# Optimization experiments

Measured on AMD Instinct MI355X. Metric: run time of the kernel, lower is better.

The kernel has to match this reference:

```python
import jax, jax.numpy as jnp
import numpy as np

B, S, N = 16, 512, 321          # batch, input length, n_variates (dec_in)
D, DF, LAYERS = 512, 2048, 2    # d_model, d_ff, e_layers
M, K, P = 3, 3, 96              # wavelet levels, kernel_size, pred_len
ALPHA = 0.3


def _dwconv(x, h, dilation):
    # x: [B, C, L], h: [C, K] depthwise dilated conv (cross-correlation, like torch)
    return jax.lax.conv_general_dilated(
        x, h[:, None, :], window_strides=(1,), padding='VALID',
        rhs_dilation=(dilation,), dimension_numbers=('NCH', 'OIH', 'NCH'),
        feature_group_count=x.shape[1])


def _swt_dec(x, h0, h1):
    # stationary wavelet decomposition; x: [B, N, D] -> [B, N, M+1, D]
    approx, coeffs, dil = x, [], 1
    for _ in range(M):
        pad_total = dil * (K - 1)
        pad_r = (K * dil) // 2
        xp = jnp.pad(approx, ((0, 0), (0, 0), (pad_total - pad_r, pad_r)), mode='wrap')
        coeffs.append(_dwconv(xp, h1, dil))
        approx = _dwconv(xp, h0, dil)
        dil *= 2
    coeffs.append(approx)
    return jnp.stack(coeffs[::-1], axis=-2)


def _swt_rec(c, g0, g1):
    # inverse SWT; c: [B, N, M+1, D] -> [B, N, D]
    approx = c[:, :, 0, :]
    dil = 2 ** (M - 1)
    for i in range(M):
        det = c[:, :, 1 + i, :]
        pad_total = dil * (K - 1)
        pad_l = (dil * K) // 2
        pads = ((0, 0), (0, 0), (pad_l, pad_total - pad_l))
        approx = (_dwconv(jnp.pad(approx, pads, mode='wrap'), g0, dil)
                  + _dwconv(jnp.pad(det, pads, mode='wrap'), g1, dil)) / 2
        dil //= 2
    return approx


def _geom_attention(q, k, v):
    # q,k,v: [B, L=D, H=M+1, E=N]
    scale = 1.0 / jnp.sqrt(jnp.float32(q.shape[-1]))
    dot = jnp.einsum('blhe,bshe->bhls', q, k)
    qn2 = jnp.sum(q * q, -1).transpose(0, 2, 1)  # [B,H,L]
    kn2 = jnp.sum(k * k, -1).transpose(0, 2, 1)  # [B,H,S]
    wedge = jnp.sqrt(jax.nn.relu(qn2[:, :, :, None] * kn2[:, :, None, :] - dot * dot) + 1e-8)
    scores = ((1.0 - ALPHA) * dot + ALPHA * wedge) * scale
    A = jax.nn.softmax(scores, axis=-1)
    return jnp.einsum('bhls,bshd->blhd', A, v)


def _layernorm(x, g, b, eps=1e-5):
    mu = x.mean(-1, keepdims=True)
    var = jnp.mean((x - mu) ** 2, -1, keepdims=True)
    return (x - mu) / jnp.sqrt(var + eps) * g + b


def _forward(x_enc, emb_W, emb_b, h0, h1, g0, g1, Wq, bq, Wk, bk, Wv, bv, Wo, bo,
             W1, b1, W2, b2, ln1_g, ln1_b, ln2_g, ln2_b, lnf_g, lnf_b, proj_W, proj_b):
    # RevIN-style normalize (means detached as in torch code)
    means = jax.lax.stop_gradient(x_enc.mean(1, keepdims=True))
    stdev = jnp.sqrt(x_enc.var(1, keepdims=True) + 1e-5)
    x = (x_enc - means) / stdev
    # inverted embedding: each variate's full series -> d_model token
    h = jnp.einsum('bsn,ds->bnd', x, emb_W) + emb_b  # [B,N,D]
    for l in range(LAYERS):
        coeffs = _swt_dec(h, h0[l], h1[l])  # [B,N,M+1,D]
        q = (jnp.einsum('bnmd,ed->bnme', coeffs, Wq[l]) + bq[l]).transpose(0, 3, 2, 1)
        kk = (jnp.einsum('bnmd,ed->bnme', coeffs, Wk[l]) + bk[l]).transpose(0, 3, 2, 1)
        vv = (jnp.einsum('bnmd,ed->bnme', coeffs, Wv[l]) + bv[l]).transpose(0, 3, 2, 1)
        out = _geom_attention(q, kk, vv).transpose(0, 3, 2, 1)  # [B,N,M+1,D]
        out = _swt_rec(out, g0[l], g1[l])                        # [B,N,D]
        out = jnp.einsum('bnd,ed->bne', out, Wo[l]) + bo[l]
        x1 = _layernorm(h + out, ln1_g[l], ln1_b[l])
        y = jax.nn.gelu(jnp.einsum('bnd,fd->bnf', x1, W1[l]) + b1[l], approximate=False)
        y = jnp.einsum('bnf,df->bnd', y, W2[l]) + b2[l]
        h = _layernorm(x1 + y, ln2_g[l], ln2_b[l])
    h = _layernorm(h, lnf_g, lnf_b)
    dec = (jnp.einsum('bnd,pd->bnp', h, proj_W) + proj_b).transpose(0, 2, 1)  # [B,P,N]
    dec = dec * stdev[:, 0, :][:, None, :] + means[:, 0, :][:, None, :]
    return dec, means, stdev


def setup_inputs():
    key = jax.random.key(0)
    ks = jax.random.split(key, 24)
    def filt(k):
        f = jax.random.normal(k, (LAYERS, N, K), jnp.float32)
        return f / jnp.linalg.norm(f, axis=-1, keepdims=True)
    w = lambda k, shape: jax.random.normal(k, shape, jnp.float32) * 0.02
    z = lambda shape: jnp.zeros(shape, jnp.float32)
    o = lambda shape: jnp.ones(shape, jnp.float32)
    return {
        'x_enc': jax.random.normal(ks[0], (B, S, N), jnp.float32),
        'emb_W': w(ks[1], (D, S)), 'emb_b': z((D,)),
        'h0': filt(ks[2]), 'h1': filt(ks[3]), 'g0': filt(ks[4]), 'g1': filt(ks[5]),
        'Wq': w(ks[6], (LAYERS, D, D)), 'bq': z((LAYERS, D)),
        'Wk': w(ks[7], (LAYERS, D, D)), 'bk': z((LAYERS, D)),
        'Wv': w(ks[8], (LAYERS, D, D)), 'bv': z((LAYERS, D)),
        'Wo': w(ks[9], (LAYERS, D, D)), 'bo': z((LAYERS, D)),
        'W1': w(ks[10], (LAYERS, DF, D)), 'b1': z((LAYERS, DF)),
        'W2': w(ks[11], (LAYERS, D, DF)), 'b2': z((LAYERS, D)),
        'ln1_g': o((LAYERS, D)), 'ln1_b': z((LAYERS, D)),
        'ln2_g': o((LAYERS, D)), 'ln2_b': z((LAYERS, D)),
        'lnf_g': o((D,)), 'lnf_b': z((D,)),
        'proj_W': w(ks[12], (P, D)), 'proj_b': z((P,)),
    }


def reference(x_enc, emb_W, emb_b, h0, h1, g0, g1, Wq, bq, Wk, bk, Wv, bv, Wo, bo,
              W1, b1, W2, b2, ln1_g, ln1_b, ln2_g, ln2_b, lnf_g, lnf_b, proj_W, proj_b):
    return _forward(x_enc, emb_W, emb_b, h0, h1, g0, g1, Wq, bq, Wk, bk, Wv, bv, Wo, bo,
                    W1, b1, W2, b2, ln1_g, ln1_b, ln2_g, ln2_b, lnf_g, lnf_b, proj_W, proj_b)
```

## Files before the change

kernel.cpp:

```cpp
#include <hip/hip_runtime.h>
#include <hip/hip_bf16.h>
#include <math.h>
#include <stdint.h>

#define Bn 16
#define Sn 512
#define Nn 321
#define Dn 512
#define DFn 2048
#define Pn 96
#define KP 352

typedef __bf16 bf16x8 __attribute__((ext_vector_type(8)));
typedef float f32x4 __attribute__((ext_vector_type(4)));
typedef __hip_bfloat16 bf16;

static __device__ __forceinline__ float gelu_exact(float x) {
    return 0.5f * x * (1.0f + erff(x * 0.7071067811865476f));
}

static __device__ __forceinline__ void gld16(const void* g, void* l) {
    __builtin_amdgcn_global_load_lds(
        (const __attribute__((address_space(1))) void*)(uintptr_t)g,
        (__attribute__((address_space(3))) void*)(uintptr_t)l, 16, 0, 0);
}

struct CvtPack {
    const float* src[14];
    bf16* dst[14];
    int cnt[14];
};
__global__ void cvt_all_kernel(CvtPack p) {
    int seg = blockIdx.y;
    int n = p.cnt[seg];
    const float* s = p.src[seg];
    bf16* d = p.dst[seg];
    int i = (blockIdx.x * 256 + threadIdx.x) * 4;
    if (i + 3 < n) {
        float4 v = *reinterpret_cast<const float4*>(s + i);
        d[i] = __float2bfloat16(v.x);
        d[i + 1] = __float2bfloat16(v.y);
        d[i + 2] = __float2bfloat16(v.z);
        d[i + 3] = __float2bfloat16(v.w);
    }
}

__global__ void bias_pack_kernel(const float* __restrict__ bq, const float* __restrict__ bk,
                                 float* __restrict__ bqk) {
    int idx = blockIdx.x * 256 + threadIdx.x;
    if (idx >= 2048) return;
    int l = idx >> 10, j = idx & 1023;
    bqk[idx] = (j < 512) ? bq[l * 512 + j] : bk[l * 512 + j - 512];
}

__global__ void stats_kernel(const float* __restrict__ x, float* __restrict__ means,
                             float* __restrict__ stdev) {
    int b = blockIdx.y;
    int n = blockIdx.x * 256 + threadIdx.x;
    if (n >= Nn) return;
    const float* p = x + (size_t)b * Sn * Nn + n;
    float s = 0.f, s2 = 0.f;
    for (int ss = 0; ss < Sn; ++ss) { float v = p[(size_t)ss * Nn]; s += v; s2 += v * v; }
    float mu = s * (1.0f / Sn);
    float var = s2 * (1.0f / Sn) - mu * mu;
    means[b * Nn + n] = mu;
    stdev[b * Nn + n] = sqrtf(var + 1e-5f);
}

__global__ void transpose_norm_kernel(const float* __restrict__ x,
                                      const float* __restrict__ means,
                                      const float* __restrict__ stdev,
                                      bf16* __restrict__ xT) {
    __shared__ float tile[32][33];
    int b = blockIdx.z;
    int s0 = blockIdx.x * 32, n0 = blockIdx.y * 32;
    int tx = threadIdx.x, ty = threadIdx.y;
#pragma unroll
    for (int u = 0; u < 4; ++u) {
        int srow = ty + u * 8;
        int n = n0 + tx;
        tile[srow][tx] = (n < Nn) ? x[((size_t)b * Sn + (s0 + srow)) * Nn + n] : 0.f;
    }
    __syncthreads();
#pragma unroll
    for (int u = 0; u < 4; ++u) {
        int n = n0 + ty + u * 8;
        int s = s0 + tx;
        if (n < Nn) {
            float mu = means[b * Nn + n], sd = stdev[b * Nn + n];
            xT[((size_t)b * Nn + n) * Sn + s] = __float2bfloat16((tile[tx][ty + u * 8] - mu) / sd);
        }
    }
}

template <int OUT, int EPI>
__global__ __launch_bounds__(256) void mm_kernel(
    const bf16* __restrict__ A, const bf16* __restrict__ Bm,
    const float* __restrict__ bias, void* __restrict__ C,
    int Mdim, int Ndim, int Kdim, int lda, int ldb, int ldc,
    long sAi, long sAo, long sBi, long sBo, long sCi, long sCo, int innerB) {
    int z = blockIdx.z;
    int zi = z % innerB, zo = z / innerB;
    const bf16* Ab = A + (size_t)zi * sAi + (size_t)zo * sAo;
    const bf16* Bb = Bm + (size_t)zi * sBi + (size_t)zo * sBo;

    int gx = gridDim.x, gy = gridDim.y;
    int lin = blockIdx.y * gx + blockIdx.x;
    int prefix = (gy & ~7) * gx;
    int bx, by;
    if (lin < prefix) {
        bx = (lin >> 3) % gx;
        by = (lin / (8 * gx)) * 8 + (lin & 7);
    } else {
        int r = lin - prefix;
        bx = r % gx;
        by = (gy & ~7) + r / gx;
    }

    __shared__ __align__(16) bf16 As[2][128 * 32];
    __shared__ __align__(16) bf16 Bs[2][128 * 32];
    int t = threadIdx.x;
    int wave = t >> 6, lane = t & 63;
    int wr = wave >> 1, wc = wave & 1;
    int q = lane >> 4, l16 = lane & 15;
    int i0 = by * 128, j0 = bx * 128;

    int srow0 = t >> 2;
    int scol = (t & 3) * 8;
    f32x4 acc[4][4] = {};

    int nIter = Kdim >> 5;

    auto stage = [&](int k0, int buf) {
#pragma unroll
        for (int u = 0; u < 2; ++u) {
            int row = u * 64 + srow0;
            int gcol = scol ^ (((row >> 1) & 3) << 3);
            int gi = i0 + row; if (gi >= Mdim) gi = Mdim - 1;
            gld16(Ab + (size_t)gi * lda + k0 + gcol, &As[buf][u * 2048 + wave * 512]);
            int gj = j0 + row; if (gj >= Ndim) gj = Ndim - 1;
            gld16(Bb + (size_t)gj * ldb + k0 + gcol, &Bs[buf][u * 2048 + wave * 512]);
        }
    };

    stage(0, 0);
    for (int it = 0; it < nIter; ++it) {
        __syncthreads();
        if (it + 1 < nIter) stage((it + 1) << 5, (it + 1) & 1);
        int buf = it & 1;
        bf16x8 af[4], bfr[4];
#pragma unroll
        for (int mi = 0; mi < 4; ++mi) {
            int r = wr * 64 + mi * 16 + l16;
            int cl = (q * 8) ^ (((r >> 1) & 3) << 3);
            af[mi] = *reinterpret_cast<const bf16x8*>(&As[buf][r * 32 + cl]);
        }
#pragma unroll
        for (int ni = 0; ni < 4; ++ni) {
            int r = wc * 64 + ni * 16 + l16;
            int cl = (q * 8) ^ (((r >> 1) & 3) << 3);
            bfr[ni] = *reinterpret_cast<const bf16x8*>(&Bs[buf][r * 32 + cl]);
        }
#pragma unroll
        for (int mi = 0; mi < 4; ++mi)
#pragma unroll
            for (int ni = 0; ni < 4; ++ni)
                acc[mi][ni] = __builtin_amdgcn_mfma_f32_16x16x32_bf16(af[mi], bfr[ni], acc[mi][ni], 0, 0, 0);
    }
    size_t cbase = (size_t)zi * sCi + (size_t)zo * sCo;
#pragma unroll
    for (int mi = 0; mi < 4; ++mi) {
#pragma unroll
        for (int r = 0; r < 4; ++r) {
            int gi = i0 + wr * 64 + mi * 16 + q * 4 + r;
            if (gi >= Mdim) continue;
#pragma unroll
            for (int ni = 0; ni < 4; ++ni) {
                int gj = j0 + wc * 64 + ni * 16 + l16;
                if (gj >= Ndim) continue;
                float v = acc[mi][ni][r];
                if (bias) v += bias[gj];
                if (EPI == 1) v = gelu_exact(v);
                size_t cidx = cbase + (size_t)gi * ldc + gj;
                if (OUT == 0) ((float*)C)[cidx] = v;
                else ((bf16*)C)[cidx] = __float2bfloat16(v);
            }
        }
    }
}

__global__ __launch_bounds__(128) void swt_dec_kernel(
    const float* __restrict__ h, const float* __restrict__ h0f,
    const float* __restrict__ h1f, bf16* __restrict__ coeffs) {
    __shared__ float a[2][512];
    int b = blockIdx.y, n = blockIdx.x, t = threadIdx.x;
    const float* hrow = h + ((size_t)b * Nn + n) * Dn;
#pragma unroll
    for (int u = 0; u < 4; ++u) a[0][t + u * 128] = hrow[t + u * 128];
    float f0[3], f1[3];
#pragma unroll
    for (int k = 0; k < 3; ++k) { f0[k] = h0f[n * 3 + k]; f1[k] = h1f[n * 3 + k]; }
    __syncthreads();
    bf16* cb = coeffs + ((size_t)b * Nn + n) * 4 * Dn;
    int cur = 0;
    for (int lev = 0; lev < 3; ++lev) {
        int dil = 1 << lev;
        int pl = 2 * dil - (3 * dil) / 2;
#pragma unroll
        for (int u = 0; u < 4; ++u) {
            int d = t + u * 128;
            float dv = 0.f, av = 0.f;
#pragma unroll
            for (int k = 0; k < 3; ++k) {
                int idx = (d + k * dil - pl) & 511;
                float xv = a[cur][idx];
                dv += f1[k] * xv;
                av += f0[k] * xv;
            }
            cb[(size_t)(3 - lev) * Dn + d] = __float2bfloat16(dv);
            a[cur ^ 1][d] = av;
        }
        __syncthreads();
        cur ^= 1;
    }
#pragma unroll
    for (int u = 0; u < 4; ++u) cb[t + u * 128] = __float2bfloat16(a[cur][t + u * 128]);
}

__global__ __launch_bounds__(128) void swt_rec_kernel(
    const bf16* __restrict__ attn, const float* __restrict__ g0f,
    const float* __restrict__ g1f, bf16* __restrict__ rec) {
    __shared__ float a[2][512];
    __shared__ float det[512];
    int b = blockIdx.y, n = blockIdx.x, t = threadIdx.x;
    const bf16* base = attn + ((size_t)(b * 4) * Nn + n) * Dn;
#pragma unroll
    for (int u = 0; u < 4; ++u) a[0][t + u * 128] = __bfloat162float(base[t + u * 128]);
    float w0[3], w1[3];
#pragma unroll
    for (int k = 0; k < 3; ++k) { w0[k] = g0f[n * 3 + k]; w1[k] = g1f[n * 3 + k]; }
    int cur = 0;
    for (int i = 0; i < 3; ++i) {
        int dil = 4 >> i;
        int pl = (3 * dil) / 2;
        const bf16* drow = base + (size_t)(1 + i) * Nn * Dn;
#pragma unroll
        for (int u = 0; u < 4; ++u) det[t + u * 128] = __bfloat162float(drow[t + u * 128]);
        __syncthreads();
#pragma unroll
        for (int u = 0; u < 4; ++u) {
            int d = t + u * 128;
            float s = 0.f;
#pragma unroll
            for (int k = 0; k < 3; ++k) {
                int idx = (d + k * dil - pl) & 511;
                s += w0[k] * a[cur][idx] + w1[k] * det[idx];
            }
            a[cur ^ 1][d] = s * 0.5f;
        }
        __syncthreads();
        cur ^= 1;
    }
    bf16* out = rec + ((size_t)b * Nn + n) * Dn;
#pragma unroll
    for (int u = 0; u < 4; ++u) out[t + u * 128] = __float2bfloat16(a[cur][t + u * 128]);
}

__global__ void tconv2_kernel(const bf16* __restrict__ QK, bf16* __restrict__ QtKt) {
    __shared__ bf16 tile[32][33];
    int zz = blockIdx.z;
    int qk = zz >> 6, bm = zz & 63;
    int b = bm >> 2, m = bm & 3;
    int e0 = blockIdx.x * 32, n0 = blockIdx.y * 32;
    int tx = threadIdx.x, ty = threadIdx.y;
    const bf16* ib = QK + (size_t)b * Nn * 4096 + (size_t)m * 1024 + (size_t)qk * 512;
    bf16* ob = QtKt + (size_t)qk * 64 * 512 * KP + (size_t)bm * 512 * KP;
#pragma unroll
    for (int u = 0; u < 4; ++u) {
        int n = n0 + ty + u * 8;
        bf16 v = __float2bfloat16(0.f);
        if (n < Nn) v = ib[(size_t)n * 4096 + e0 + tx];
        tile[ty + u * 8][tx] = v;
    }
    __syncthreads();
#pragma unroll
    for (int u = 0; u < 4; ++u) {
        int e = e0 + ty + u * 8;
        int n = n0 + tx;
        if (n < KP) ob[(size_t)e * KP + n] = tile[tx][ty + u * 8];
    }
}

__global__ __launch_bounds__(256) void colsq2_kernel(const bf16* __restrict__ QK,
                                                     float* __restrict__ outv) {
    int y = blockIdx.y;
    int qk = y >> 6, bm = y & 63;
    int b = bm >> 2, m = bm & 3;
    int e0 = blockIdx.x * 64;
    int tx = threadIdx.x & 63, ty = threadIdx.x >> 6;
    const bf16* base = QK + ((size_t)b * Nn * 4 + m) * 1024 + (size_t)qk * 512;
    float s = 0.f;
    for (int n = ty; n < Nn; n += 4) {
        float v = __bfloat162float(base[(size_t)n * 4096 + e0 + tx]);
        s += v * v;
    }
    __shared__ float red[4][64];
    red[ty][tx] = s;
    __syncthreads();
    if (ty == 0)
        outv[(size_t)qk * 32768 + (size_t)bm * 512 + e0 + tx] =
            red[0][tx] + red[1][tx] + red[2][tx] + red[3][tx];
}

__global__ __launch_bounds__(256) void wedge_softmax_kernel(
    bf16* __restrict__ Smat, const float* __restrict__ qn2, const float* __restrict__ kn2) {
    int bm = blockIdx.y, l = blockIdx.x, t = threadIdx.x;
    bf16* row = Smat + ((size_t)bm * 512 + l) * 512;
    const float* kn = kn2 + (size_t)bm * 512;
    float q2 = qn2[(size_t)bm * 512 + l];
    const float scale = rsqrtf(321.0f);
    float v[2];
    float mx = -1e30f;
#pragma unroll
    for (int u = 0; u < 2; ++u) {
        int s = t + u * 256;
        float d = __bfloat162float(row[s]);
        float w = sqrtf(fmaxf(q2 * kn[s] - d * d, 0.f) + 1e-8f);
        float sc = (0.7f * d + 0.3f * w) * scale;
        v[u] = sc;
        mx = fmaxf(mx, sc);
    }
    __shared__ float red[256];
    red[t] = mx;
    __syncthreads();
    for (int o = 128; o > 0; o >>= 1) {
        if (t < o) red[t] = fmaxf(red[t], red[t + o]);
        __syncthreads();
    }
    mx = red[0];
    __syncthreads();
    float sum = 0.f;
#pragma unroll
    for (int u = 0; u < 2; ++u) {
        v[u] = expf(v[u] - mx);
        sum += v[u];
    }
    red[t] = sum;
    __syncthreads();
    for (int o = 128; o > 0; o >>= 1) {
        if (t < o) red[t] += red[t + o];
        __syncthreads();
    }
    float inv = 1.0f / red[0];
#pragma unroll
    for (int u = 0; u < 2; ++u) row[t + u * 256] = __float2bfloat16(v[u] * inv);
}

__global__ __launch_bounds__(128) void ln_kernel(
    const float* __restrict__ A, const float* __restrict__ R, const float* __restrict__ R2,
    const float* __restrict__ g, const float* __restrict__ bb,
    float* __restrict__ outf, bf16* __restrict__ outb) {
    size_t r = blockIdx.x;
    int t = threadIdx.x;
    const float* ra = A + r * Dn;
    float x[4];
    float s = 0.f, s2 = 0.f;
#pragma unroll
    for (int u = 0; u < 4; ++u) {
        int d = t + u * 128;
        float v = ra[d];
        if (R) v += R[r * Dn + d];
        if (R2) v += R2[r * Dn + d];
        x[u] = v;
        s += v;
        s2 += v * v;
    }
    __shared__ float rs[128], rs2[128];
    rs[t] = s;
    rs2[t] = s2;
    __syncthreads();
    for (int o = 64; o > 0; o >>= 1) {
        if (t < o) { rs[t] += rs[t + o]; rs2[t] += rs2[t + o]; }
        __syncthreads();
    }
    float mean = rs[0] * (1.0f / Dn);
    float var = rs2[0] * (1.0f / Dn) - mean * mean;
    float inv = rsqrtf(var + 1e-5f);
#pragma unroll
    for (int u = 0; u < 4; ++u) {
        int d = t + u * 128;
        float v = (x[u] - mean) * inv * g[d] + bb[d];
        if (outf) outf[r * Dn + d] = v;
        if (outb) outb[r * Dn + d] = __float2bfloat16(v);
    }
}

__global__ void out_scale_kernel(const float* __restrict__ ptmp,
                                 const float* __restrict__ means,
                                 const float* __restrict__ stdev, float* __restrict__ dec) {
    int idx = blockIdx.x * 256 + threadIdx.x;
    if (idx >= Bn * Pn * Nn) return;
    int n = idx % Nn;
    int bp = idx / Nn;
    int p = bp % Pn;
    int b = bp / Pn;
    const size_t PS = (size_t)Bn * Nn * Pn;
    size_t base = ((size_t)b * Nn + n) * Pn + p;
    float v = ptmp[base] + ptmp[base + PS] + ptmp[base + 2 * PS] + ptmp[base + 3 * PS];
    dec[idx] = v * stdev[b * Nn + n] + means[b * Nn + n];
}

extern "C" void kernel_launch(void* const* d_in, const int* in_sizes, int n_in,
                              void* d_out, int out_size, void* d_ws, size_t ws_size,
                              hipStream_t stream) {
    const float* x_enc = (const float*)d_in[0];
    const float* emb_W = (const float*)d_in[1];
    const float* emb_b = (const float*)d_in[2];
    const float* h0 = (const float*)d_in[3];
    const float* h1 = (const float*)d_in[4];
    const float* g0 = (const float*)d_in[5];
    const float* g1 = (const float*)d_in[6];
    const float* Wq = (const float*)d_in[7];
    const float* bq = (const float*)d_in[8];
    const float* Wk = (const float*)d_in[9];
    const float* bk = (const float*)d_in[10];
    const float* Wv = (const float*)d_in[11];
    const float* bv = (const float*)d_in[12];
    const float* Wo = (const float*)d_in[13];
    const float* bo = (const float*)d_in[14];
    const float* W1 = (const float*)d_in[15];
    const float* b1 = (const float*)d_in[16];
    const float* W2 = (const float*)d_in[17];
    const float* b2 = (const float*)d_in[18];
    const float* ln1_g = (const float*)d_in[19];
    const float* ln1_b = (const float*)d_in[20];
    const float* ln2_g = (const float*)d_in[21];
    const float* ln2_b = (const float*)d_in[22];
    const float* lnf_g = (const float*)d_in[23];
    const float* lnf_b = (const float*)d_in[24];
    const float* proj_W = (const float*)d_in[25];
    const float* proj_b = (const float*)d_in[26];

    float* dec = (float*)d_out;
    float* means = dec + (size_t)Bn * Pn * Nn;
    float* stdev = means + (size_t)Bn * Nn;

    char* p = (char*)d_ws;
    auto alloc = [&](size_t bytes) { char* r = p; p += (bytes + 255) & ~(size_t)255; return r; };
    const size_t RD = (size_t)Bn * Nn * Dn;
    const size_t RQ4 = RD * 4;

    bf16* embWb = (bf16*)alloc(262144 * 2);
    bf16* Wqkb = (bf16*)alloc(2 * 524288 * 2);
    bf16* Wvb = (bf16*)alloc(2 * 262144 * 2);
    bf16* Wob = (bf16*)alloc(2 * 262144 * 2);
    bf16* W1b = (bf16*)alloc(2 * 1048576 * 2);
    bf16* W2b = (bf16*)alloc(2 * 1048576 * 2);
    bf16* projWb = (bf16*)alloc(49152 * 2);
    float* bqk = (float*)alloc(2048 * 4);

    float* hbuf = (float*)alloc(RD * 4);
    char* regC = alloc(RQ4 * 2);
    char* regQ = alloc(RQ4 * 2);
    char* regK = alloc(RQ4 * 2);
    char* regV = alloc(RQ4 * 2);
    char* regT = alloc((size_t)2 * 64 * 512 * KP * 2);
    float* qn2 = (float*)alloc((size_t)2 * 64 * 512 * 4);
    float* kn2 = qn2 + 32768;

    bf16* coeffs_b = (bf16*)regC;
    bf16* attn_b = (bf16*)regC;
    bf16* QK0b = (bf16*)regQ;
    bf16* Smat = (bf16*)regQ;
    bf16* recb = (bf16*)regQ;
    bf16* x1b = (bf16*)(regQ + RD * 2);
    float* ptmp = (float*)regQ;
    bf16* V0b = (bf16*)regV;
    bf16* yb = (bf16*)regV;
    bf16* QtKt = (bf16*)regT;
    bf16* Qt = QtKt;
    bf16* Kt = QtKt + (size_t)64 * 512 * KP;
    bf16* xT_b = (bf16*)regT;
    float* x1 = (float*)regT;
    float* tmp = (float*)(regT + RD * 4);
    bf16* hfb = (bf16*)(regT + RD * 12);

    const int R = Bn * Nn;
    const int RQr = R * 4;
    const long sbm = (long)4 * Nn * 512;
    const long sS = (long)512 * 512;
    const long sTq = (long)512 * KP;
    const long sTb = 4 * sTq;

    CvtPack cp;
    int ci = 0;
    auto addcvt = [&](const float* s, bf16* d, int n) { cp.src[ci] = s; cp.dst[ci] = d; cp.cnt[ci] = n; ++ci; };
    addcvt(emb_W, embWb, 262144);
    for (int l = 0; l < 2; ++l) {
        addcvt(Wq + (size_t)l * 262144, Wqkb + (size_t)l * 524288, 262144);
        addcvt(Wk + (size_t)l * 262144, Wqkb + (size_t)l * 524288 + 262144, 262144);
        addcvt(Wv + (size_t)l * 262144, Wvb + (size_t)l * 262144, 262144);
        addcvt(Wo + (size_t)l * 262144, Wob + (size_t)l * 262144, 262144);
        addcvt(W1 + (size_t)l * 1048576, W1b + (size_t)l * 1048576, 1048576);
        addcvt(W2 + (size_t)l * 1048576, W2b + (size_t)l * 1048576, 1048576);
    }
    addcvt(proj_W, projWb, 49152);
    cvt_all_kernel<<<dim3(1048576 / 4 / 256, 14), 256, 0, stream>>>(cp);
    bias_pack_kernel<<<8, 256, 0, stream>>>(bq, bk, bqk);

    stats_kernel<<<dim3((Nn + 255) / 256, Bn), 256, 0, stream>>>(x_enc, means, stdev);
    transpose_norm_kernel<<<dim3(Sn / 32, (Nn + 31) / 32, Bn), dim3(32, 8), 0, stream>>>(
        x_enc, means, stdev, xT_b);

    mm_kernel<0, 0><<<dim3(4, (R + 127) / 128, 1), 256, 0, stream>>>(
        xT_b, embWb, emb_b, hbuf, R, Dn, Sn, Sn, Sn, Dn, 0, 0, 0, 0, 0, 0, 1);

    for (int l = 0; l < 2; ++l) {
        const float* h0l = h0 + (size_t)l * Nn * 3;
        const float* h1l = h1 + (size_t)l * Nn * 3;
        const float* g0l = g0 + (size_t)l * Nn * 3;
        const float* g1l = g1 + (size_t)l * Nn * 3;

        swt_dec_kernel<<<dim3(Nn, Bn), 128, 0, stream>>>(hbuf, h0l, h1l, coeffs_b);

        mm_kernel<1, 0><<<dim3(8, (RQr + 127) / 128, 1), 256, 0, stream>>>(
            coeffs_b, Wqkb + (size_t)l * 524288, bqk + (size_t)l * 1024, QK0b,
            RQr, 1024, Dn, Dn, Dn, 1024, 0, 0, 0, 0, 0, 0, 1);
        mm_kernel<1, 0><<<dim3(4, (RQr + 127) / 128, 1), 256, 0, stream>>>(
            coeffs_b, Wvb + (size_t)l * 262144, bv + (size_t)l * Dn, V0b,
            RQr, Dn, Dn, Dn, Dn, Dn, 0, 0, 0, 0, 0, 0, 1);

        colsq2_kernel<<<dim3(8, 128), 256, 0, stream>>>(QK0b, qn2);
        tconv2_kernel<<<dim3(16, 11, 128), dim3(32, 8), 0, stream>>>(QK0b, QtKt);

        mm_kernel<1, 0><<<dim3(4, 4, 64), 256, 0, stream>>>(
            Qt, Kt, nullptr, Smat, 512, 512, KP, KP, KP, 512,
            sTq, sTb, sTq, sTb, sS, 4 * sS, 4);

        wedge_softmax_kernel<<<dim3(512, 64), 256, 0, stream>>>(Smat, qn2, kn2);

        mm_kernel<1, 0><<<dim3(4, (Nn + 127) / 128, 64), 256, 0, stream>>>(
            V0b, Smat, nullptr, attn_b, Nn, 512, 512, 2048, 512, 512,
            512, sbm, sS, 4 * sS, (long)Nn * 512, (long)4 * Nn * 512, 4);

        swt_rec_kernel<<<dim3(Nn, Bn), 128, 0, stream>>>(attn_b, g0l, g1l, recb);

        mm_kernel<0, 0><<<dim3(4, (R + 127) / 128, 2), 256, 0, stream>>>(
            recb, Wob + (size_t)l * 262144, bo + (size_t)l * Dn, tmp,
            R, Dn, 256, Dn, Dn, Dn, 256, 0, 256, 0, (long)RD, 0, 2);
        ln_kernel<<<R, 128, 0, stream>>>(hbuf, tmp, tmp + RD, ln1_g + (size_t)l * Dn,
                                         ln1_b + (size_t)l * Dn, x1, x1b);

        mm_kernel<1, 1><<<dim3(16, (R + 127) / 128, 1), 256, 0, stream>>>(
            x1b, W1b + (size_t)l * 1048576, b1 + (size_t)l * DFn, yb,
            R, DFn, Dn, Dn, Dn, DFn, 0, 0, 0, 0, 0, 0, 1);
        mm_kernel<0, 0><<<dim3(4, (R + 127) / 128, 2), 256, 0, stream>>>(
            yb, W2b + (size_t)l * 1048576, b2 + (size_t)l * Dn, tmp,
            R, Dn, 1024, DFn, DFn, Dn, 1024, 0, 1024, 0, (long)RD, 0, 2);
        ln_kernel<<<R, 128, 0, stream>>>(x1, tmp, tmp + RD, ln2_g + (size_t)l * Dn,
                                         ln2_b + (size_t)l * Dn, hbuf, nullptr);
    }

    ln_kernel<<<R, 128, 0, stream>>>(hbuf, nullptr, nullptr, lnf_g, lnf_b, nullptr, hfb);
    mm_kernel<0, 0><<<dim3(1, (R + 127) / 128, 4), 256, 0, stream>>>(
        hfb, projWb, proj_b, ptmp, R, Pn, 128, Dn, Dn, Pn,
        128, 0, 128, 0, (long)R * Pn, 0, 4);
    out_scale_kernel<<<(Bn * Pn * Nn + 255) / 256, 256, 0, stream>>>(ptmp, means, stdev, dec);
}
```

Baseline: 914.8 us.

## Add 256-row GEMM tiles, wave-per-row softmax/layernorm, and colsq from transposed buffer

Templates the GEMM on the M tile size and uses 256-row tiles for the QK projection and the score GEMM, giving more reuse of B per block at the cost of more registers and LDS. Softmax and layernorm now use one wave per row with vectorized loads and shuffle reductions in place of block-wide shared-memory reductions. Column squared norms are computed from the contiguous transposed QtKt buffer instead of strided reads of QK0b. The larger tiles may lower occupancy and leave fewer blocks for some grids. The ln_kernel launch assumes R is divisible by 4.

```diff
diff --git a/kernel.cpp b/kernel.cpp
--- a/kernel.cpp
+++ b/kernel.cpp
@@ -93,7 +93,7 @@
     }
 }
 
-template <int OUT, int EPI>
+template <int MT, int OUT, int EPI>
 __global__ __launch_bounds__(256) void mm_kernel(
     const bf16* __restrict__ A, const bf16* __restrict__ Bm,
     const float* __restrict__ bias, void* __restrict__ C,
@@ -117,27 +117,34 @@
         by = (gy & ~7) + r / gx;
     }
 
-    __shared__ __align__(16) bf16 As[2][128 * 32];
+    constexpr int MI = MT / 32;
+    constexpr int AR = MT / 64;
+    __shared__ __align__(16) bf16 As[2][MT * 32];
     __shared__ __align__(16) bf16 Bs[2][128 * 32];
     int t = threadIdx.x;
     int wave = t >> 6, lane = t & 63;
     int wr = wave >> 1, wc = wave & 1;
     int q = lane >> 4, l16 = lane & 15;
-    int i0 = by * 128, j0 = bx * 128;
+    int i0 = by * MT, j0 = bx * 128;
 
     int srow0 = t >> 2;
     int scol = (t & 3) * 8;
-    f32x4 acc[4][4] = {};
+    f32x4 acc[MI][4] = {};
 
     int nIter = Kdim >> 5;
 
     auto stage = [&](int k0, int buf) {
 #pragma unroll
-        for (int u = 0; u < 2; ++u) {
+        for (int u = 0; u < AR; ++u) {
             int row = u * 64 + srow0;
             int gcol = scol ^ (((row >> 1) & 3) << 3);
             int gi = i0 + row; if (gi >= Mdim) gi = Mdim - 1;
             gld16(Ab + (size_t)gi * lda + k0 + gcol, &As[buf][u * 2048 + wave * 512]);
+        }
+#pragma unroll
+        for (int u = 0; u < 2; ++u) {
+            int row = u * 64 + srow0;
+            int gcol = scol ^ (((row >> 1) & 3) << 3);
             int gj = j0 + row; if (gj >= Ndim) gj = Ndim - 1;
             gld16(Bb + (size_t)gj * ldb + k0 + gcol, &Bs[buf][u * 2048 + wave * 512]);
         }
@@ -148,10 +155,10 @@
         __syncthreads();
         if (it + 1 < nIter) stage((it + 1) << 5, (it + 1) & 1);
         int buf = it & 1;
-        bf16x8 af[4], bfr[4];
-#pragma unroll
-        for (int mi = 0; mi < 4; ++mi) {
-            int r = wr * 64 + mi * 16 + l16;
+        bf16x8 af[MI], bfr[4];
+#pragma unroll
+        for (int mi = 0; mi < MI; ++mi) {
+            int r = wr * (MT / 2) + mi * 16 + l16;
             int cl = (q * 8) ^ (((r >> 1) & 3) << 3);
             af[mi] = *reinterpret_cast<const bf16x8*>(&As[buf][r * 32 + cl]);
         }
@@ -162,17 +169,17 @@
             bfr[ni] = *reinterpret_cast<const bf16x8*>(&Bs[buf][r * 32 + cl]);
         }
 #pragma unroll
-        for (int mi = 0; mi < 4; ++mi)
+        for (int mi = 0; mi < MI; ++mi)
 #pragma unroll
             for (int ni = 0; ni < 4; ++ni)
                 acc[mi][ni] = __builtin_amdgcn_mfma_f32_16x16x32_bf16(af[mi], bfr[ni], acc[mi][ni], 0, 0, 0);
     }
     size_t cbase = (size_t)zi * sCi + (size_t)zo * sCo;
 #pragma unroll
-    for (int mi = 0; mi < 4; ++mi) {
+    for (int mi = 0; mi < MI; ++mi) {
 #pragma unroll
         for (int r = 0; r < 4; ++r) {
-            int gi = i0 + wr * 64 + mi * 16 + q * 4 + r;
+            int gi = i0 + wr * (MT / 2) + mi * 16 + q * 4 + r;
             if (gi >= Mdim) continue;
 #pragma unroll
             for (int ni = 0; ni < 4; ++ni) {
@@ -291,105 +298,96 @@
     }
 }
 
-__global__ __launch_bounds__(256) void colsq2_kernel(const bf16* __restrict__ QK,
-                                                     float* __restrict__ outv) {
-    int y = blockIdx.y;
-    int qk = y >> 6, bm = y & 63;
-    int b = bm >> 2, m = bm & 3;
-    int e0 = blockIdx.x * 64;
-    int tx = threadIdx.x & 63, ty = threadIdx.x >> 6;
-    const bf16* base = QK + ((size_t)b * Nn * 4 + m) * 1024 + (size_t)qk * 512;
+__global__ __launch_bounds__(256) void colsq_t_kernel(const bf16* __restrict__ QtKt,
+                                                      float* __restrict__ outv) {
+    int wave = threadIdx.x >> 6, lane = threadIdx.x & 63;
+    size_t row = (size_t)blockIdx.x * 4 + wave;
+    const bf16* p = QtKt + row * KP;
     float s = 0.f;
-    for (int n = ty; n < Nn; n += 4) {
-        float v = __bfloat162float(base[(size_t)n * 4096 + e0 + tx]);
-        s += v * v;
-    }
-    __shared__ float red[4][64];
-    red[ty][tx] = s;
-    __syncthreads();
-    if (ty == 0)
-        outv[(size_t)qk * 32768 + (size_t)bm * 512 + e0 + tx] =
-            red[0][tx] + red[1][tx] + red[2][tx] + red[3][tx];
+#pragma unroll
+    for (int j = 0; j < 6; ++j) {
+        int idx = lane + j * 64;
+        if (idx < KP) { float v = __bfloat162float(p[idx]); s += v * v; }
+    }
+#pragma unroll
+    for (int m = 1; m < 64; m <<= 1) s += __shfl_xor(s, m);
+    if (lane == 0) outv[row] = s;
 }
 
 __global__ __launch_bounds__(256) void wedge_softmax_kernel(
     bf16* __restrict__ Smat, const float* __restrict__ qn2, const float* __restrict__ kn2) {
-    int bm = blockIdx.y, l = blockIdx.x, t = threadIdx.x;
-    bf16* row = Smat + ((size_t)bm * 512 + l) * 512;
+    int wave = threadIdx.x >> 6, lane = threadIdx.x & 63;
+    int rowid = blockIdx.x * 4 + wave;
+    int bm = rowid >> 9, l = rowid & 511;
+    bf16* row = Smat + (size_t)rowid * 512;
     const float* kn = kn2 + (size_t)bm * 512;
     float q2 = qn2[(size_t)bm * 512 + l];
     const float scale = rsqrtf(321.0f);
-    float v[2];
+    bf16x8 dv = *reinterpret_cast<const bf16x8*>(row + lane * 8);
+    float kk[8];
+    *reinterpret_cast<float4*>(&kk[0]) = *reinterpret_cast<const float4*>(kn + lane * 8);
+    *reinterpret_cast<float4*>(&kk[4]) = *reinterpret_cast<const float4*>(kn + lane * 8 + 4);
+    float sc[8];
     float mx = -1e30f;
 #pragma unroll
-    for (int u = 0; u < 2; ++u) {
-        int s = t + u * 256;
-        float d = __bfloat162float(row[s]);
-        float w = sqrtf(fmaxf(q2 * kn[s] - d * d, 0.f) + 1e-8f);
-        float sc = (0.7f * d + 0.3f * w) * scale;
-        v[u] = sc;
-        mx = fmaxf(mx, sc);
-    }
-    __shared__ float red[256];
-    red[t] = mx;
-    __syncthreads();
-    for (int o = 128; o > 0; o >>= 1) {
-        if (t < o) red[t] = fmaxf(red[t], red[t + o]);
-        __syncthreads();
-    }
-    mx = red[0];
-    __syncthreads();
+    for (int j = 0; j < 8; ++j) {
+        float d = (float)dv[j];
+        float w = sqrtf(fmaxf(q2 * kk[j] - d * d, 0.f) + 1e-8f);
+        sc[j] = (0.7f * d + 0.3f * w) * scale;
+        mx = fmaxf(mx, sc[j]);
+    }
+#pragma unroll
+    for (int m = 1; m < 64; m <<= 1) mx = fmaxf(mx, __shfl_xor(mx, m));
     float sum = 0.f;
 #pragma unroll
-    for (int u = 0; u < 2; ++u) {
-        v[u] = expf(v[u] - mx);
-        sum += v[u];
-    }
-    red[t] = sum;
-    __syncthreads();
-    for (int o = 128; o > 0; o >>= 1) {
-        if (t < o) red[t] += red[t + o];
-        __syncthreads();
-    }
-    float inv = 1.0f / red[0];
-#pragma unroll
-    for (int u = 0; u < 2; ++u) row[t + u * 256] = __float2bfloat16(v[u] * inv);
-}
-
-__global__ __launch_bounds__(128) void ln_kernel(
+    for (int j = 0; j < 8; ++j) { sc[j] = expf(sc[j] - mx); sum += sc[j]; }
+#pragma unroll
+    for (int m = 1; m < 64; m <<= 1) sum += __shfl_xor(sum, m);
+    float inv = 1.0f / sum;
+    bf16x8 o;
+#pragma unroll
+    for (int j = 0; j < 8; ++j) o[j] = (__bf16)(sc[j] * inv);
+    *reinterpret_cast<bf16x8*>(row + lane * 8) = o;
+}
+
+__global__ __launch_bounds__(256) void ln_kernel(
     const float* __restrict__ A, const float* __restrict__ R, const float* __restrict__ R2,
     const float* __restrict__ g, const float* __restrict__ bb,
     float* __restrict__ outf, bf16* __restrict__ outb) {
-    size_t r = blockIdx.x;
-    int t = threadIdx.x;
-    const float* ra = A + r * Dn;
-    float x[4];
+    int wave = threadIdx.x >> 6, lane = threadIdx.x & 63;
+    size_t r = (size_t)blockIdx.x * 4 + wave;
+    const float* ra = A + r * Dn + lane * 8;
+    float x[8];
+    *reinterpret_cast<float4*>(&x[0]) = *reinterpret_cast<const float4*>(ra);
+    *reinterpret_cast<float4*>(&x[4]) = *reinterpret_cast<const float4*>(ra + 4);
+    if (R) {
+        const float* rr = R + r * Dn + lane * 8;
+        float y[8];
+        *reinterpret_cast<float4*>(&y[0]) = *reinterpret_cast<const float4*>(rr);
+        *reinterpret_cast<float4*>(&y[4]) = *reinterpret_cast<const float4*>(rr + 4);
+#pragma unroll
+        for (int j = 0; j < 8; ++j) x[j] += y[j];
+    }
+    if (R2) {
+        const float* rr = R2 + r * Dn + lane * 8;
+        float y[8];
+        *reinterpret_cast<float4*>(&y[0]) = *reinterpret_cast<const float4*>(rr);
+        *reinterpret_cast<float4*>(&y[4]) = *reinterpret_cast<const float4*>(rr + 4);
+#pragma unroll
+        for (int j = 0; j < 8; ++j) x[j] += y[j];
+    }
     float s = 0.f, s2 = 0.f;
 #pragma unroll
-    for (int u = 0; u < 4; ++u) {
-        int d = t + u * 128;
-        float v = ra[d];
-        if (R) v += R[r * Dn + d];
-        if (R2) v += R2[r * Dn + d];
-        x[u] = v;
-        s += v;
-        s2 += v * v;
-    }
-    __shared__ float rs[128], rs2[128];
-    rs[t] = s;
-    rs2[t] = s2;
-    __syncthreads();
-    for (int o = 64; o > 0; o >>= 1) {
-        if (t < o) { rs[t] += rs[t + o]; rs2[t] += rs2[t + o]; }
-        __syncthreads();
-    }
-    float mean = rs[0] * (1.0f / Dn);
-    float var = rs2[0] * (1.0f / Dn) - mean * mean;
+    for (int j = 0; j < 8; ++j) { s += x[j]; s2 += x[j] * x[j]; }
+#pragma unroll
+    for (int m = 1; m < 64; m <<= 1) { s += __shfl_xor(s, m); s2 += __shfl_xor(s2, m); }
+    float mean = s * (1.0f / Dn);
+    float var = s2 * (1.0f / Dn) - mean * mean;
     float inv = rsqrtf(var + 1e-5f);
 #pragma unroll
-    for (int u = 0; u < 4; ++u) {
-        int d = t + u * 128;
-        float v = (x[u] - mean) * inv * g[d] + bb[d];
+    for (int j = 0; j < 8; ++j) {
+        int d = lane * 8 + j;
+        float v = (x[j] - mean) * inv * g[d] + bb[d];
         if (outf) outf[r * Dn + d] = v;
         if (outb) outb[r * Dn + d] = __float2bfloat16(v);
     }
@@ -512,7 +510,7 @@
     transpose_norm_kernel<<<dim3(Sn / 32, (Nn + 31) / 32, Bn), dim3(32, 8), 0, stream>>>(
         x_enc, means, stdev, xT_b);
 
-    mm_kernel<0, 0><<<dim3(4, (R + 127) / 128, 1), 256, 0, stream>>>(
+    mm_kernel<128, 0, 0><<<dim3(4, (R + 127) / 128, 1), 256, 0, stream>>>(
         xT_b, embWb, emb_b, hbuf, R, Dn, Sn, Sn, Sn, Dn, 0, 0, 0, 0, 0, 0, 1);
 
     for (int l = 0; l < 2; ++l) {
@@ -523,46 +521,46 @@
 
         swt_dec_kernel<<<dim3(Nn, Bn), 128, 0, stream>>>(hbuf, h0l, h1l, coeffs_b);
 
-        mm_kernel<1, 0><<<dim3(8, (RQr + 127) / 128, 1), 256, 0, stream>>>(
+        mm_kernel<256, 1, 0><<<dim3(8, (RQr + 255) / 256, 1), 256, 0, stream>>>(
             coeffs_b, Wqkb + (size_t)l * 524288, bqk + (size_t)l * 1024, QK0b,
             RQr, 1024, Dn, Dn, Dn, 1024, 0, 0, 0, 0, 0, 0, 1);
-        mm_kernel<1, 0><<<dim3(4, (RQr + 127) / 128, 1), 256, 0, stream>>>(
+        mm_kernel<128, 1, 0><<<dim3(4, (RQr + 127) / 128, 1), 256, 0, stream>>>(
             coeffs_b, Wvb + (size_t)l * 262144, bv + (size_t)l * Dn, V0b,
             RQr, Dn, Dn, Dn, Dn, Dn, 0, 0, 0, 0, 0, 0, 1);
 
-        colsq2_kernel<<<dim3(8, 128), 256, 0, stream>>>(QK0b, qn2);
         tconv2_kernel<<<dim3(16, 11, 128), dim3(32, 8), 0, stream>>>(QK0b, QtKt);
-
-        mm_kernel<1, 0><<<dim3(4, 4, 64), 256, 0, stream>>>(
+        colsq_t_kernel<<<16384, 256, 0, stream>>>(QtKt, qn2);
+
+        mm_kernel<256, 1, 0><<<dim3(4, 2, 64), 256, 0, stream>>>(
             Qt, Kt, nullptr, Smat, 512, 512, KP, KP, KP, 512,
             sTq, sTb, sTq, sTb, sS, 4 * sS, 4);
 
-        wedge_softmax_kernel<<<dim3(512, 64), 256, 0, stream>>>(Smat, qn2, kn2);
-
-        mm_kernel<1, 0><<<dim3(4, (Nn + 127) / 128, 64), 256, 0, stream>>>(
+        wedge_softmax_kernel<<<8192, 256, 0, stream>>>(Smat, qn2, kn2);
+
+        mm_kernel<128, 1, 0><<<dim3(4, (Nn + 127) / 128, 64), 256, 0, stream>>>(
             V0b, Smat, nullptr, attn_b, Nn, 512, 512, 2048, 512, 512,
             512, sbm, sS, 4 * sS, (long)Nn * 512, (long)4 * Nn * 512, 4);
 
         swt_rec_kernel<<<dim3(Nn, Bn), 128, 0, stream>>>(attn_b, g0l, g1l, recb);
 
-        mm_kernel<0, 0><<<dim3(4, (R + 127) / 128, 2), 256, 0, stream>>>(
+        mm_kernel<128, 0, 0><<<dim3(4, (R + 127) / 128, 2), 256, 0, stream>>>(
             recb, Wob + (size_t)l * 262144, bo + (size_t)l * Dn, tmp,
             R, Dn, 256, Dn, Dn, Dn, 256, 0, 256, 0, (long)RD, 0, 2);
-        ln_kernel<<<R, 128, 0, stream>>>(hbuf, tmp, tmp + RD, ln1_g + (size_t)l * Dn,
-                                         ln1_b + (size_t)l * Dn, x1, x1b);
-
-        mm_kernel<1, 1><<<dim3(16, (R + 127) / 128, 1), 256, 0, stream>>>(
+        ln_kernel<<<R / 4, 256, 0, stream>>>(hbuf, tmp, tmp + RD, ln1_g + (size_t)l * Dn,
+                                             ln1_b + (size_t)l * Dn, x1, x1b);
+
+        mm_kernel<128, 1, 1><<<dim3(16, (R + 127) / 128, 1), 256, 0, stream>>>(
             x1b, W1b + (size_t)l * 1048576, b1 + (size_t)l * DFn, yb,
             R, DFn, Dn, Dn, Dn, DFn, 0, 0, 0, 0, 0, 0, 1);
-        mm_kernel<0, 0><<<dim3(4, (R + 127) / 128, 2), 256, 0, stream>>>(
+        mm_kernel<128, 0, 0><<<dim3(4, (R + 127) / 128, 2), 256, 0, stream>>>(
             yb, W2b + (size_t)l * 1048576, b2 + (size_t)l * Dn, tmp,
             R, Dn, 1024, DFn, DFn, Dn, 1024, 0, 1024, 0, (long)RD, 0, 2);
-        ln_kernel<<<R, 128, 0, stream>>>(x1, tmp, tmp + RD, ln2_g + (size_t)l * Dn,
-                                         ln2_b + (size_t)l * Dn, hbuf, nullptr);
-    }
-
-    ln_kernel<<<R, 128, 0, stream>>>(hbuf, nullptr, nullptr, lnf_g, lnf_b, nullptr, hfb);
-    mm_kernel<0, 0><<<dim3(1, (R + 127) / 128, 4), 256, 0, stream>>>(
+        ln_kernel<<<R / 4, 256, 0, stream>>>(x1, tmp, tmp + RD, ln2_g + (size_t)l * Dn,
+                                             ln2_b + (size_t)l * Dn, hbuf, nullptr);
+    }
+
+    ln_kernel<<<R / 4, 256, 0, stream>>>(hbuf, nullptr, nullptr, lnf_g, lnf_b, nullptr, hfb);
+    mm_kernel<128, 0, 0><<<dim3(1, (R + 127) / 128, 4), 256, 0, stream>>>(
         hfb, projWb, proj_b, ptmp, R, Pn, 128, Dn, Dn, Pn,
         128, 0, 128, 0, (long)R * Pn, 0, 4);
     out_scale_kernel<<<(Bn * Pn * Nn + 255) / 256, 256, 0, stream>>>(ptmp, means, stdev, dec);
```

Measured after the change: 997.0 us. 9.0% more time.
